# Optimization experiments

Hardware: AMD Instinct MI355X
Metric: run time of the kernel (lower is better)

Reference implementation:

```python
import jax, jax.numpy as jnp
import numpy as np

N_EMBED = 384
T_MAX = 256
EPS = 1e-5


def layer_norm(x, gamma, beta):
    mu = jnp.mean(x, axis=-1, keepdims=True)
    var = jnp.mean(jnp.square(x - mu), axis=-1, keepdims=True)
    return (x - mu) * jax.lax.rsqrt(var + EPS) * gamma + beta


def setup_inputs() -> dict:
    key = jax.random.key(0)
    ks = jax.random.split(key, 12)
    B, T, C = 128, 256, N_EMBED
    s = lambda fan_in: 1.0 / np.sqrt(fan_in)
    return {
        "x": jax.random.normal(ks[0], (B, T, C), dtype=jnp.float32),
        "W_attn": jax.random.uniform(ks[1], (C, 3 * C), minval=-s(C), maxval=s(C), dtype=jnp.float32),
        "b_attn": jax.random.uniform(ks[2], (3 * C,), minval=-s(C), maxval=s(C), dtype=jnp.float32),
        "W_proj": jax.random.uniform(ks[3], (C, C), minval=-s(C), maxval=s(C), dtype=jnp.float32),
        "b_proj": jax.random.uniform(ks[4], (C,), minval=-s(C), maxval=s(C), dtype=jnp.float32),
        "ln1_g": jnp.ones((C,), jnp.float32),
        "ln1_b": jnp.zeros((C,), jnp.float32),
        "ln2_g": jnp.ones((C,), jnp.float32),
        "ln2_b": jnp.zeros((C,), jnp.float32),
        "W1": jax.random.uniform(ks[5], (C, 4 * C), minval=-s(C), maxval=s(C), dtype=jnp.float32),
        "b1": jax.random.uniform(ks[6], (4 * C,), minval=-s(C), maxval=s(C), dtype=jnp.float32),
        "W2": jax.random.uniform(ks[7], (4 * C, C), minval=-s(4 * C), maxval=s(4 * C), dtype=jnp.float32),
        "b2": jax.random.uniform(ks[8], (4 * C,)[:1] and (C,), minval=-s(4 * C), maxval=s(4 * C), dtype=jnp.float32),
    }


def reference(x, W_attn, b_attn, W_proj, b_proj, ln1_g, ln1_b, ln2_g, ln2_b, W1, b1, W2, b2):
    B, T, C = x.shape
    # --- pre-LN single-head causal self-attention ---
    h = layer_norm(x, ln1_g, ln1_b)
    qkv = h @ W_attn + b_attn                      # [B,T,3C]
    q, k, v = jnp.split(qkv, 3, axis=-1)           # each [B,T,C]
    att = jnp.einsum('btc,bsc->bts', q, k) * (1.0 / jnp.sqrt(jnp.float32(C)))
    causal = jnp.tril(jnp.ones((T, T), bool))
    att = jnp.where(causal, att, -jnp.inf)
    att = jax.nn.softmax(att, axis=-1)             # dropout is identity (eval)
    y = jnp.einsum('bts,bsc->btc', att, v)
    x = x + (y @ W_proj + b_proj)
    # --- pre-LN MLP ---
    h2 = layer_norm(x, ln2_g, ln2_b)
    x = x + (jax.nn.relu(h2 @ W1 + b1) @ W2 + b2)
    return x
```

## Files before the change

kernel.cpp:

```cpp
#include <hip/hip_runtime.h>
#include <hip/hip_bf16.h>

#define C_EMB 384
#define T_SEQ 256
#define B_BATCH 128
#define M_ROWS (B_BATCH * T_SEQ)
#define QKV_LD 1152
#define BK 64

typedef __bf16 bf16_8 __attribute__((ext_vector_type(8)));
typedef float f32x4 __attribute__((ext_vector_type(4)));

__device__ __forceinline__ void load16_lds(const __bf16* g, __bf16* l) {
    __builtin_amdgcn_global_load_lds(
        (const __attribute__((address_space(1))) unsigned int*)g,
        (__attribute__((address_space(3))) unsigned int*)l, 16, 0, 0);
}

__global__ __launch_bounds__(256) void cast_all_kernel(const float* __restrict__ Wa,
                                                       const float* __restrict__ Wp,
                                                       const float* __restrict__ W1,
                                                       const float* __restrict__ W2,
                                                       __bf16* __restrict__ Wa_t,
                                                       __bf16* __restrict__ Wp_t,
                                                       __bf16* __restrict__ W1_t,
                                                       __bf16* __restrict__ W2_t) {
    int bid = blockIdx.x;
    const float* W; __bf16* Wt; int K, N, tx_n;
    if (bid < 432)      { W = Wa; Wt = Wa_t; K = 384;  N = 1152; tx_n = 36; }
    else if (bid < 576) { bid -= 432; W = Wp; Wt = Wp_t; K = 384;  N = 384;  tx_n = 12; }
    else if (bid < 1152){ bid -= 576; W = W1; Wt = W1_t; K = 384;  N = 1536; tx_n = 48; }
    else                { bid -= 1152; W = W2; Wt = W2_t; K = 1536; N = 384;  tx_n = 12; }
    int n0 = (bid % tx_n) * 32, k0 = (bid / tx_n) * 32;

    __shared__ float t[32][33];
    int tx = threadIdx.x & 31, ty = threadIdx.x >> 5;
#pragma unroll
    for (int i = 0; i < 4; ++i)
        t[ty + i * 8][tx] = W[(size_t)(k0 + ty + i * 8) * N + n0 + tx];
    __syncthreads();
#pragma unroll
    for (int i = 0; i < 4; ++i) {
        int n = ty + i * 8;
        Wt[(size_t)(n0 + n) * K + k0 + tx] = (__bf16)t[tx][n];
    }
}

__global__ __launch_bounds__(384) void ln_kernel(const float* __restrict__ x,
                                                 const float* __restrict__ g,
                                                 const float* __restrict__ bta,
                                                 __bf16* __restrict__ out) {
    int row = blockIdx.x;
    int c = threadIdx.x;
    float v = x[(size_t)row * C_EMB + c];

    __shared__ float red[6];
    float s = v;
#pragma unroll
    for (int o = 32; o; o >>= 1) s += __shfl_down(s, o);
    if ((c & 63) == 0) red[c >> 6] = s;
    __syncthreads();
    float mu = (red[0] + red[1] + red[2] + red[3] + red[4] + red[5]) * (1.0f / C_EMB);

    float d = v - mu;
    float s2 = d * d;
#pragma unroll
    for (int o = 32; o; o >>= 1) s2 += __shfl_down(s2, o);
    __syncthreads();
    if ((c & 63) == 0) red[c >> 6] = s2;
    __syncthreads();
    float var = (red[0] + red[1] + red[2] + red[3] + red[4] + red[5]) * (1.0f / C_EMB);

    out[(size_t)row * C_EMB + c] = (__bf16)(d * rsqrtf(var + 1e-5f) * g[c] + bta[c]);
}

template <int TM, bool RELU, bool RESID, bool OUT_BF16>
__global__ __launch_bounds__(256) void mfma_gemm(const __bf16* __restrict__ A, int lda,
                                                 const __bf16* __restrict__ Bt, int ldb,
                                                 const float* __restrict__ bias,
                                                 const float* __restrict__ resid,
                                                 void* __restrict__ out_,
                                                 int N, int K) {
    constexpr int MI = TM / 32;
    constexpr int WROWS = TM / 2;
    __shared__ __align__(16) __bf16 As[2 * TM * 32];
    __shared__ __align__(16) __bf16 Bs[2 * 128 * 32];

    int tid = threadIdx.x;
    int wave = tid >> 6, lane = tid & 63;
    int wr = wave >> 1, wc = wave & 1;
    int quad = lane >> 4, l16 = lane & 15;
    int bm = blockIdx.y * TM, bn = blockIdx.x * 128;
    int lrow = lane >> 2, lcol = (lane & 3) * 8;

    f32x4 acc[MI][4] = {};

    for (int k0 = 0; k0 < K; k0 += BK) {
        const __bf16* Ab = A + (size_t)bm * lda + k0;
        const __bf16* Bb = Bt + (size_t)bn * ldb + k0;
#pragma unroll
        for (int p = 0; p < 2; ++p) {
#pragma unroll
            for (int i = 0; i < TM / 64; ++i) {
                int r0 = (i * 4 + wave) * 16;
                load16_lds(Ab + (size_t)(r0 + lrow) * lda + p * 32 + lcol,
                           &As[p * TM * 32 + r0 * 32]);
            }
#pragma unroll
            for (int i = 0; i < 2; ++i) {
                int r0 = (i * 4 + wave) * 16;
                load16_lds(Bb + (size_t)(r0 + lrow) * ldb + p * 32 + lcol,
                           &Bs[p * 128 * 32 + r0 * 32]);
            }
        }
        __syncthreads();

        bf16_8 af[MI][2], bf[4][2];
#pragma unroll
        for (int p = 0; p < 2; ++p) {
#pragma unroll
            for (int i = 0; i < MI; ++i)
                af[i][p] = *reinterpret_cast<const bf16_8*>(
                    &As[p * TM * 32 + (wr * WROWS + i * 16 + l16) * 32 + quad * 8]);
#pragma unroll
            for (int j = 0; j < 4; ++j)
                bf[j][p] = *reinterpret_cast<const bf16_8*>(
                    &Bs[p * 128 * 32 + (wc * 64 + j * 16 + l16) * 32 + quad * 8]);
        }
#pragma unroll
        for (int i = 0; i < MI; ++i)
#pragma unroll
            for (int j = 0; j < 4; ++j) {
                acc[i][j] = __builtin_amdgcn_mfma_f32_16x16x32_bf16(af[i][0], bf[j][0], acc[i][j], 0, 0, 0);
                acc[i][j] = __builtin_amdgcn_mfma_f32_16x16x32_bf16(af[i][1], bf[j][1], acc[i][j], 0, 0, 0);
            }
        __syncthreads();
    }

#pragma unroll
    for (int i = 0; i < MI; ++i) {
#pragma unroll
        for (int r = 0; r < 4; ++r) {
            int m = bm + wr * WROWS + i * 16 + quad * 4 + r;
#pragma unroll
            for (int j = 0; j < 4; ++j) {
                int n = bn + wc * 64 + j * 16 + l16;
                float v = acc[i][j][r] + bias[n];
                if (RELU) v = fmaxf(v, 0.0f);
                if (RESID) v += resid[(size_t)m * N + n];
                if (OUT_BF16)
                    ((__bf16*)out_)[(size_t)m * N + n] = (__bf16)v;
                else
                    ((float*)out_)[(size_t)m * N + n] = v;
            }
        }
    }
}

__global__ __launch_bounds__(256) void proj_ln_kernel(const __bf16* __restrict__ A,
                                                      const __bf16* __restrict__ Bt,
                                                      const float* __restrict__ bias,
                                                      const float* __restrict__ resid,
                                                      const float* __restrict__ lng,
                                                      const float* __restrict__ lnb,
                                                      float* __restrict__ out,
                                                      __bf16* __restrict__ h) {
    __shared__ __align__(16) __bf16 As[2 * 64 * 32];
    __shared__ __align__(16) __bf16 Bs[2 * 384 * 32];
    __shared__ float red[2][2][64];

    int tid = threadIdx.x;
    int wave = tid >> 6, lane = tid & 63;
    int wr = wave >> 1, wc = wave & 1;
    int quad = lane >> 4, l16 = lane & 15;
    int bm = blockIdx.x * 64;
    int lrow = lane >> 2, lcol = (lane & 3) * 8;

    f32x4 acc[2][12] = {};

    for (int k0 = 0; k0 < C_EMB; k0 += BK) {
        const __bf16* Ab = A + (size_t)bm * C_EMB + k0;
        const __bf16* Bb = Bt + k0;
#pragma unroll
        for (int p = 0; p < 2; ++p) {
            {
                int r0 = wave * 16;
                load16_lds(Ab + (size_t)(r0 + lrow) * C_EMB + p * 32 + lcol,
                           &As[p * 64 * 32 + r0 * 32]);
            }
#pragma unroll
            for (int i = 0; i < 6; ++i) {
                int r0 = (i * 4 + wave) * 16;
                load16_lds(Bb + (size_t)(r0 + lrow) * C_EMB + p * 32 + lcol,
                           &Bs[p * 384 * 32 + r0 * 32]);
            }
        }
        __syncthreads();

        bf16_8 af[2][2], bf[12][2];
#pragma unroll
        for (int p = 0; p < 2; ++p) {
#pragma unroll
            for (int i = 0; i < 2; ++i)
                af[i][p] = *reinterpret_cast<const bf16_8*>(
                    &As[p * 64 * 32 + (wr * 32 + i * 16 + l16) * 32 + quad * 8]);
#pragma unroll
            for (int j = 0; j < 12; ++j)
                bf[j][p] = *reinterpret_cast<const bf16_8*>(
                    &Bs[p * 384 * 32 + (wc * 192 + j * 16 + l16) * 32 + quad * 8]);
        }
#pragma unroll
        for (int i = 0; i < 2; ++i)
#pragma unroll
            for (int j = 0; j < 12; ++j) {
                acc[i][j] = __builtin_amdgcn_mfma_f32_16x16x32_bf16(af[i][0], bf[j][0], acc[i][j], 0, 0, 0);
                acc[i][j] = __builtin_amdgcn_mfma_f32_16x16x32_bf16(af[i][1], bf[j][1], acc[i][j], 0, 0, 0);
            }
        __syncthreads();
    }

    float bia[12], gg[12], bb[12];
#pragma unroll
    for (int j = 0; j < 12; ++j) {
        int n = wc * 192 + j * 16 + l16;
        bia[j] = bias[n];
        gg[j] = lng[n];
        bb[j] = lnb[n];
    }

#pragma unroll
    for (int i = 0; i < 2; ++i)
#pragma unroll
        for (int r = 0; r < 4; ++r) {
            int rloc = wr * 32 + i * 16 + quad * 4 + r;
            int m = bm + rloc;
            float s = 0.0f, s2 = 0.0f;
#pragma unroll
            for (int j = 0; j < 12; ++j) {
                int n = wc * 192 + j * 16 + l16;
                float v = acc[i][j][r] + bia[j] + resid[(size_t)m * C_EMB + n];
                acc[i][j][r] = v;
                s += v;
                s2 += v * v;
            }
#pragma unroll
            for (int o = 8; o; o >>= 1) {
                s += __shfl_xor(s, o);
                s2 += __shfl_xor(s2, o);
            }
            if (l16 == 0) {
                red[0][wc][rloc] = s;
                red[1][wc][rloc] = s2;
            }
        }
    __syncthreads();

#pragma unroll
    for (int i = 0; i < 2; ++i)
#pragma unroll
        for (int r = 0; r < 4; ++r) {
            int rloc = wr * 32 + i * 16 + quad * 4 + r;
            int m = bm + rloc;
            float mu  = (red[0][0][rloc] + red[0][1][rloc]) * (1.0f / C_EMB);
            float ex2 = (red[1][0][rloc] + red[1][1][rloc]) * (1.0f / C_EMB);
            float rstd = rsqrtf(ex2 - mu * mu + 1e-5f);
#pragma unroll
            for (int j = 0; j < 12; ++j) {
                int n = wc * 192 + j * 16 + l16;
                float v = acc[i][j][r];
                out[(size_t)m * C_EMB + n] = v;
                h[(size_t)m * C_EMB + n] = (__bf16)((v - mu) * rstd * gg[j] + bb[j]);
            }
        }
}

__global__ __launch_bounds__(256) void vt_kernel(const __bf16* __restrict__ qkv,
                                                 __bf16* __restrict__ Vt) {
    __shared__ __align__(16) __bf16 t[32][72];
    int b = blockIdx.z, c0 = blockIdx.x * 64, s0 = blockIdx.y * 32;
    int tid = threadIdx.x;

    int tx = tid & 7, ty = tid >> 3;
    const __bf16* src = qkv + ((size_t)b * T_SEQ + s0 + ty) * QKV_LD + 768 + c0 + tx * 8;
    *reinterpret_cast<float4*>(&t[ty][tx * 8]) = *reinterpret_cast<const float4*>(src);
    __syncthreads();

    int sx = tid & 3, cy = tid >> 2;
    __align__(16) __bf16 tmp[8];
#pragma unroll
    for (int j = 0; j < 8; ++j) tmp[j] = t[sx * 8 + j][cy];
    *reinterpret_cast<float4*>(&Vt[((size_t)b * C_EMB + c0 + cy) * T_SEQ + s0 + sx * 8]) =
        *reinterpret_cast<float4*>(tmp);
}

__global__ __launch_bounds__(256) void qks_mfma(const __bf16* __restrict__ qkv,
                                                __bf16* __restrict__ P) {
    int b = blockIdx.y;
    int bx = blockIdx.x;
    int bm = bx * 128;
    int ntiles = bx + 1;
    const __bf16* Ab0 = qkv + (size_t)b * T_SEQ * QKV_LD;
    const __bf16* Bb0 = Ab0 + 384;

    __shared__ __align__(16) __bf16 As[2 * 128 * 32];
    __shared__ __align__(16) __bf16 Bs[2 * 128 * 32];
    __shared__ float red[2][2][128];

    int tid = threadIdx.x;
    int wave = tid >> 6, lane = tid & 63;
    int wr = wave >> 1, wc = wave & 1;
    int quad = lane >> 4, l16 = lane & 15;
    int lrow = lane >> 2, lcol = (lane & 3) * 8;

    f32x4 acc[2][4][4] = {};

#pragma unroll
    for (int nt = 0; nt < 2; ++nt) {
        if (nt < ntiles) {
            int bn = nt * 128;
            for (int k0 = 0; k0 < C_EMB; k0 += BK) {
                const __bf16* Ab = Ab0 + (size_t)bm * QKV_LD + k0;
                const __bf16* Bb = Bb0 + (size_t)bn * QKV_LD + k0;
#pragma unroll
                for (int p = 0; p < 2; ++p)
#pragma unroll
                    for (int i = 0; i < 2; ++i) {
                        int r0 = (i * 4 + wave) * 16;
                        load16_lds(Ab + (size_t)(r0 + lrow) * QKV_LD + p * 32 + lcol,
                                   &As[p * 128 * 32 + r0 * 32]);
                        load16_lds(Bb + (size_t)(r0 + lrow) * QKV_LD + p * 32 + lcol,
                                   &Bs[p * 128 * 32 + r0 * 32]);
                    }
                __syncthreads();

                bf16_8 af[4][2], bf[4][2];
#pragma unroll
                for (int p = 0; p < 2; ++p)
#pragma unroll
                    for (int i = 0; i < 4; ++i) {
                        af[i][p] = *reinterpret_cast<const bf16_8*>(
                            &As[p * 128 * 32 + (wr * 64 + i * 16 + l16) * 32 + quad * 8]);
                        bf[i][p] = *reinterpret_cast<const bf16_8*>(
                            &Bs[p * 128 * 32 + (wc * 64 + i * 16 + l16) * 32 + quad * 8]);
                    }
#pragma unroll
                for (int i = 0; i < 4; ++i)
#pragma unroll
                    for (int j = 0; j < 4; ++j) {
                        acc[nt][i][j] = __builtin_amdgcn_mfma_f32_16x16x32_bf16(af[i][0], bf[j][0], acc[nt][i][j], 0, 0, 0);
                        acc[nt][i][j] = __builtin_amdgcn_mfma_f32_16x16x32_bf16(af[i][1], bf[j][1], acc[nt][i][j], 0, 0, 0);
                    }
                __syncthreads();
            }
        }
    }

    const float scale = 0.05103103630798288f;

#pragma unroll
    for (int i = 0; i < 4; ++i)
#pragma unroll
        for (int r = 0; r < 4; ++r) {
            int rloc = wr * 64 + i * 16 + quad * 4 + r;
            int t = bm + rloc;
            float m = -INFINITY;
#pragma unroll
            for (int nt = 0; nt < 2; ++nt)
#pragma unroll
                for (int j = 0; j < 4; ++j) {
                    int n = nt * 128 + wc * 64 + j * 16 + l16;
                    bool ok = (nt < ntiles) && (n <= t);
                    float v = acc[nt][i][j][r] * scale;
                    m = fmaxf(m, ok ? v : -INFINITY);
                }
#pragma unroll
            for (int o = 8; o; o >>= 1) m = fmaxf(m, __shfl_xor(m, o));
            if (l16 == 0) red[0][wc][rloc] = m;
        }
    __syncthreads();

#pragma unroll
    for (int i = 0; i < 4; ++i)
#pragma unroll
        for (int r = 0; r < 4; ++r) {
            int rloc = wr * 64 + i * 16 + quad * 4 + r;
            int t = bm + rloc;
            float M = fmaxf(red[0][0][rloc], red[0][1][rloc]);
            float s = 0.0f;
#pragma unroll
            for (int nt = 0; nt < 2; ++nt)
#pragma unroll
                for (int j = 0; j < 4; ++j) {
                    int n = nt * 128 + wc * 64 + j * 16 + l16;
                    bool ok = (nt < ntiles) && (n <= t);
                    float p = ok ? __expf(acc[nt][i][j][r] * scale - M) : 0.0f;
                    acc[nt][i][j][r] = p;
                    s += p;
                }
#pragma unroll
            for (int o = 8; o; o >>= 1) s += __shfl_xor(s, o);
            if (l16 == 0) red[1][wc][rloc] = s;
        }
    __syncthreads();

    __bf16* Pb_ = P + (size_t)b * T_SEQ * T_SEQ;
#pragma unroll
    for (int i = 0; i < 4; ++i)
#pragma unroll
        for (int r = 0; r < 4; ++r) {
            int rloc = wr * 64 + i * 16 + quad * 4 + r;
            float inv = 1.0f / (red[1][0][rloc] + red[1][1][rloc]);
#pragma unroll
            for (int nt = 0; nt < 2; ++nt)
                if (nt < ntiles)
#pragma unroll
                    for (int j = 0; j < 4; ++j) {
                        int n = nt * 128 + wc * 64 + j * 16 + l16;
                        Pb_[(size_t)(bm + rloc) * T_SEQ + n] = (__bf16)(acc[nt][i][j][r] * inv);
                    }
        }
}

__global__ __launch_bounds__(256) void pv_mfma(const __bf16* __restrict__ P,
                                               const __bf16* __restrict__ Vt,
                                               __bf16* __restrict__ y) {
    int b = blockIdx.z;
    int bm = blockIdx.y * 128, bn = blockIdx.x * 128;
    const __bf16* Ab0 = P + (size_t)b * T_SEQ * T_SEQ;
    const __bf16* Bb0 = Vt + (size_t)b * C_EMB * T_SEQ;

    __shared__ __align__(16) __bf16 As[2 * 128 * 32];
    __shared__ __align__(16) __bf16 Bs[2 * 128 * 32];

    int tid = threadIdx.x;
    int wave = tid >> 6, lane = tid & 63;
    int wr = wave >> 1, wc = wave & 1;
    int quad = lane >> 4, l16 = lane & 15;
    int lrow = lane >> 2, lcol = (lane & 3) * 8;

    f32x4 acc[4][4] = {};

    int kmax = bm + 128;
    for (int k0 = 0; k0 < kmax; k0 += BK) {
        const __bf16* Ab = Ab0 + (size_t)bm * T_SEQ + k0;
        const __bf16* Bb = Bb0 + (size_t)bn * T_SEQ + k0;
#pragma unroll
        for (int p = 0; p < 2; ++p)
#pragma unroll
            for (int i = 0; i < 2; ++i) {
                int r0 = (i * 4 + wave) * 16;
                load16_lds(Ab + (size_t)(r0 + lrow) * T_SEQ + p * 32 + lcol,
                           &As[p * 128 * 32 + r0 * 32]);
                load16_lds(Bb + (size_t)(r0 + lrow) * T_SEQ + p * 32 + lcol,
                           &Bs[p * 128 * 32 + r0 * 32]);
            }
        __syncthreads();

        bf16_8 af[4][2], bf[4][2];
#pragma unroll
        for (int p = 0; p < 2; ++p)
#pragma unroll
            for (int i = 0; i < 4; ++i) {
                af[i][p] = *reinterpret_cast<const bf16_8*>(
                    &As[p * 128 * 32 + (wr * 64 + i * 16 + l16) * 32 + quad * 8]);
                bf[i][p] = *reinterpret_cast<const bf16_8*>(
                    &Bs[p * 128 * 32 + (wc * 64 + i * 16 + l16) * 32 + quad * 8]);
            }
#pragma unroll
        for (int i = 0; i < 4; ++i)
#pragma unroll
            for (int j = 0; j < 4; ++j) {
                acc[i][j] = __builtin_amdgcn_mfma_f32_16x16x32_bf16(af[i][0], bf[j][0], acc[i][j], 0, 0, 0);
                acc[i][j] = __builtin_amdgcn_mfma_f32_16x16x32_bf16(af[i][1], bf[j][1], acc[i][j], 0, 0, 0);
            }
        __syncthreads();
    }

#pragma unroll
    for (int i = 0; i < 4; ++i) {
#pragma unroll
        for (int r = 0; r < 4; ++r) {
            int m = bm + wr * 64 + i * 16 + quad * 4 + r;
#pragma unroll
            for (int j = 0; j < 4; ++j) {
                int n = bn + wc * 64 + j * 16 + l16;
                y[((size_t)b * T_SEQ + m) * C_EMB + n] = (__bf16)acc[i][j][r];
            }
        }
    }
}

extern "C" void kernel_launch(void* const* d_in, const int* in_sizes, int n_in,
                              void* d_out, int out_size, void* d_ws, size_t ws_size,
                              hipStream_t stream) {
    const float* x      = (const float*)d_in[0];
    const float* W_attn = (const float*)d_in[1];
    const float* b_attn = (const float*)d_in[2];
    const float* W_proj = (const float*)d_in[3];
    const float* b_proj = (const float*)d_in[4];
    const float* ln1_g  = (const float*)d_in[5];
    const float* ln1_b  = (const float*)d_in[6];
    const float* ln2_g  = (const float*)d_in[7];
    const float* ln2_b  = (const float*)d_in[8];
    const float* W1     = (const float*)d_in[9];
    const float* b1     = (const float*)d_in[10];
    const float* W2     = (const float*)d_in[11];
    const float* b2     = (const float*)d_in[12];
    float* out = (float*)d_out;

    __bf16* Wattn_t = (__bf16*)d_ws;
    __bf16* Wproj_t = Wattn_t + (size_t)1152 * 384;
    __bf16* W1_t    = Wproj_t + (size_t)384 * 384;
    __bf16* W2_t    = W1_t + (size_t)1536 * 384;
    __bf16* h       = W2_t + (size_t)384 * 1536;
    __bf16* yb      = h + (size_t)M_ROWS * 384;
    __bf16* qkv     = yb + (size_t)M_ROWS * 384;
    float*  S       = (float*)(qkv + (size_t)M_ROWS * QKV_LD);
    __bf16* Pb      = (__bf16*)(S + (size_t)B_BATCH * T_SEQ * T_SEQ);
    __bf16* Vt      = Pb + (size_t)B_BATCH * T_SEQ * T_SEQ;
    __bf16* ff      = qkv;

    cast_all_kernel<<<1728, 256, 0, stream>>>(W_attn, W_proj, W1, W2,
                                              Wattn_t, Wproj_t, W1_t, W2_t);

    ln_kernel<<<M_ROWS, 384, 0, stream>>>(x, ln1_g, ln1_b, h);
    mfma_gemm<128, false, false, true><<<dim3(1152 / 128, M_ROWS / 128), 256, 0, stream>>>(
        h, 384, Wattn_t, 384, b_attn, nullptr, qkv, 1152, 384);
    vt_kernel<<<dim3(C_EMB / 64, T_SEQ / 32, B_BATCH), 256, 0, stream>>>(qkv, Vt);
    qks_mfma<<<dim3(2, B_BATCH), 256, 0, stream>>>(qkv, Pb);
    pv_mfma<<<dim3(C_EMB / 128, T_SEQ / 128, B_BATCH), 256, 0, stream>>>(Pb, Vt, yb);
    proj_ln_kernel<<<M_ROWS / 64, 256, 0, stream>>>(yb, Wproj_t, b_proj, x,
                                                    ln2_g, ln2_b, out, h);
    mfma_gemm<128, true, false, true><<<dim3(1536 / 128, M_ROWS / 128), 256, 0, stream>>>(
        h, 384, W1_t, 384, b1, nullptr, ff, 1536, 384);
    mfma_gemm<64, false, true, false><<<dim3(384 / 128, M_ROWS / 64), 256, 0, stream>>>(
        ff, 1536, W2_t, 1536, b2, out, out, 384, 1536);
}
```

Before: 469.9 us.

## Replace GEMM kernel with double-buffered 128x384 tile pipelined MFMA GEMM

Replaces the generic MFMA GEMM with a 512-thread kernel that computes 128x384 output tiles. It double-buffers LDS so global-to-LDS loads for the next K step overlap the MFMAs on the current one, and it XOR-swizzles the LDS layout to avoid bank conflicts. Each block reuses a wider B tile, which cuts A re-reads and uses one barrier per K step. The cost is heavy LDS use (about 128KB), which limits occupancy to one block per CU, plus a large register footprint, and the W2 GEMM launches only 256 blocks.

```diff
diff --git a/kernel.cpp b/kernel.cpp
--- a/kernel.cpp
+++ b/kernel.cpp
@@ -74,87 +74,95 @@
     out[(size_t)row * C_EMB + c] = (__bf16)(d * rsqrtf(var + 1e-5f) * g[c] + bta[c]);
 }
 
-template <int TM, bool RELU, bool RESID, bool OUT_BF16>
-__global__ __launch_bounds__(256) void mfma_gemm(const __bf16* __restrict__ A, int lda,
-                                                 const __bf16* __restrict__ Bt, int ldb,
-                                                 const float* __restrict__ bias,
-                                                 const float* __restrict__ resid,
-                                                 void* __restrict__ out_,
-                                                 int N, int K) {
-    constexpr int MI = TM / 32;
-    constexpr int WROWS = TM / 2;
-    __shared__ __align__(16) __bf16 As[2 * TM * 32];
-    __shared__ __align__(16) __bf16 Bs[2 * 128 * 32];
+template <int K, int NFULL, bool RELU, bool ACCUM>
+__global__ __launch_bounds__(512, 1) void gemm_pipe(const __bf16* __restrict__ A,
+                                                    const __bf16* __restrict__ Bt,
+                                                    const float* __restrict__ bias,
+                                                    void* __restrict__ out_) {
+    __shared__ __align__(16) __bf16 At[2][128 * 64];
+    __shared__ __align__(16) __bf16 Bs[2][384 * 64];
 
     int tid = threadIdx.x;
     int wave = tid >> 6, lane = tid & 63;
-    int wr = wave >> 1, wc = wave & 1;
+    int wr = wave >> 2, wc = wave & 3;
     int quad = lane >> 4, l16 = lane & 15;
-    int bm = blockIdx.y * TM, bn = blockIdx.x * 128;
-    int lrow = lane >> 2, lcol = (lane & 3) * 8;
-
-    f32x4 acc[MI][4] = {};
-
-    for (int k0 = 0; k0 < K; k0 += BK) {
-        const __bf16* Ab = A + (size_t)bm * lda + k0;
-        const __bf16* Bb = Bt + (size_t)bn * ldb + k0;
-#pragma unroll
-        for (int p = 0; p < 2; ++p) {
-#pragma unroll
-            for (int i = 0; i < TM / 64; ++i) {
-                int r0 = (i * 4 + wave) * 16;
-                load16_lds(Ab + (size_t)(r0 + lrow) * lda + p * 32 + lcol,
-                           &As[p * TM * 32 + r0 * 32]);
-            }
-#pragma unroll
-            for (int i = 0; i < 2; ++i) {
-                int r0 = (i * 4 + wave) * 16;
-                load16_lds(Bb + (size_t)(r0 + lrow) * ldb + p * 32 + lcol,
-                           &Bs[p * 128 * 32 + r0 * 32]);
-            }
-        }
-        __syncthreads();
-
-        bf16_8 af[MI][2], bf[4][2];
-#pragma unroll
-        for (int p = 0; p < 2; ++p) {
-#pragma unroll
-            for (int i = 0; i < MI; ++i)
-                af[i][p] = *reinterpret_cast<const bf16_8*>(
-                    &As[p * TM * 32 + (wr * WROWS + i * 16 + l16) * 32 + quad * 8]);
-#pragma unroll
-            for (int j = 0; j < 4; ++j)
-                bf[j][p] = *reinterpret_cast<const bf16_8*>(
-                    &Bs[p * 128 * 32 + (wc * 64 + j * 16 + l16) * 32 + quad * 8]);
-        }
-#pragma unroll
-        for (int i = 0; i < MI; ++i)
-#pragma unroll
-            for (int j = 0; j < 4; ++j) {
-                acc[i][j] = __builtin_amdgcn_mfma_f32_16x16x32_bf16(af[i][0], bf[j][0], acc[i][j], 0, 0, 0);
-                acc[i][j] = __builtin_amdgcn_mfma_f32_16x16x32_bf16(af[i][1], bf[j][1], acc[i][j], 0, 0, 0);
-            }
-        __syncthreads();
-    }
-
-#pragma unroll
-    for (int i = 0; i < MI; ++i) {
-#pragma unroll
-        for (int r = 0; r < 4; ++r) {
-            int m = bm + wr * WROWS + i * 16 + quad * 4 + r;
-#pragma unroll
-            for (int j = 0; j < 4; ++j) {
-                int n = bn + wc * 64 + j * 16 + l16;
+    int bm = blockIdx.y * 128;
+    int n0 = blockIdx.x * 384;
+    int srow = lane >> 3;
+    int sunit = (lane & 7) ^ srow;
+
+    const __bf16* asrc0 = A + (size_t)(bm + srow) * K + sunit * 8;
+    const __bf16* bsrc0 = Bt + (size_t)(n0 + srow) * K + sunit * 8;
+
+    auto stage = [&](int buf, int k0) {
+#pragma unroll
+        for (int t = 0; t < 2; ++t) {
+            int g = t * 8 + wave;
+            load16_lds(asrc0 + (size_t)(g * 8) * K + k0, &At[buf][g * 8 * 64]);
+        }
+#pragma unroll
+        for (int t = 0; t < 6; ++t) {
+            int g = t * 8 + wave;
+            load16_lds(bsrc0 + (size_t)(g * 8) * K + k0, &Bs[buf][g * 8 * 64]);
+        }
+    };
+
+    f32x4 acc[4][6] = {};
+
+    stage(0, 0);
+    asm volatile("s_waitcnt vmcnt(0)" ::: "memory");
+    __builtin_amdgcn_sched_barrier(0);
+    __builtin_amdgcn_s_barrier();
+
+#pragma unroll 2
+    for (int kt = 0; kt < K / BK; ++kt) {
+        int cur = kt & 1;
+        if (kt < K / BK - 1) stage(cur ^ 1, (kt + 1) * BK);
+
+        bf16_8 af[4][2];
+#pragma unroll
+        for (int p = 0; p < 2; ++p)
+#pragma unroll
+            for (int i = 0; i < 4; ++i) {
+                int row = wr * 64 + i * 16 + l16;
+                int u = (p * 4 + quad) ^ (row & 7);
+                af[i][p] = *reinterpret_cast<const bf16_8*>(&At[cur][row * 64 + u * 8]);
+            }
+#pragma unroll
+        for (int p = 0; p < 2; ++p)
+#pragma unroll
+            for (int j = 0; j < 6; ++j) {
+                int row = wc * 96 + j * 16 + l16;
+                int u = (p * 4 + quad) ^ (row & 7);
+                bf16_8 bf = *reinterpret_cast<const bf16_8*>(&Bs[cur][row * 64 + u * 8]);
+#pragma unroll
+                for (int i = 0; i < 4; ++i)
+                    acc[i][j] = __builtin_amdgcn_mfma_f32_16x16x32_bf16(af[i][p], bf, acc[i][j], 0, 0, 0);
+            }
+
+        asm volatile("s_waitcnt vmcnt(0)" ::: "memory");
+        __builtin_amdgcn_sched_barrier(0);
+        __builtin_amdgcn_s_barrier();
+    }
+
+#pragma unroll
+    for (int i = 0; i < 4; ++i)
+#pragma unroll
+        for (int r = 0; r < 4; ++r) {
+            int m = bm + wr * 64 + i * 16 + quad * 4 + r;
+#pragma unroll
+            for (int j = 0; j < 6; ++j) {
+                int n = n0 + wc * 96 + j * 16 + l16;
                 float v = acc[i][j][r] + bias[n];
                 if (RELU) v = fmaxf(v, 0.0f);
-                if (RESID) v += resid[(size_t)m * N + n];
-                if (OUT_BF16)
-                    ((__bf16*)out_)[(size_t)m * N + n] = (__bf16)v;
-                else
-                    ((float*)out_)[(size_t)m * N + n] = v;
-            }
-        }
-    }
+                if (ACCUM) {
+                    float* o = &((float*)out_)[(size_t)m * NFULL + n];
+                    *o = *o + v;
+                } else {
+                    ((__bf16*)out_)[(size_t)m * NFULL + n] = (__bf16)v;
+                }
+            }
+        }
 }
 
 __global__ __launch_bounds__(256) void proj_ln_kernel(const __bf16* __restrict__ A,
@@ -524,15 +532,15 @@
                                               Wattn_t, Wproj_t, W1_t, W2_t);
 
     ln_kernel<<<M_ROWS, 384, 0, stream>>>(x, ln1_g, ln1_b, h);
-    mfma_gemm<128, false, false, true><<<dim3(1152 / 128, M_ROWS / 128), 256, 0, stream>>>(
-        h, 384, Wattn_t, 384, b_attn, nullptr, qkv, 1152, 384);
+    gemm_pipe<384, 1152, false, false><<<dim3(1152 / 384, M_ROWS / 128), 512, 0, stream>>>(
+        h, Wattn_t, b_attn, qkv);
     vt_kernel<<<dim3(C_EMB / 64, T_SEQ / 32, B_BATCH), 256, 0, stream>>>(qkv, Vt);
     qks_mfma<<<dim3(2, B_BATCH), 256, 0, stream>>>(qkv, Pb);
     pv_mfma<<<dim3(C_EMB / 128, T_SEQ / 128, B_BATCH), 256, 0, stream>>>(Pb, Vt, yb);
     proj_ln_kernel<<<M_ROWS / 64, 256, 0, stream>>>(yb, Wproj_t, b_proj, x,
                                                     ln2_g, ln2_b, out, h);
-    mfma_gemm<128, true, false, true><<<dim3(1536 / 128, M_ROWS / 128), 256, 0, stream>>>(
-        h, 384, W1_t, 384, b1, nullptr, ff, 1536, 384);
-    mfma_gemm<64, false, true, false><<<dim3(384 / 128, M_ROWS / 64), 256, 0, stream>>>(
-        ff, 1536, W2_t, 1536, b2, out, out, 384, 1536);
-}
+    gemm_pipe<384, 1536, true, false><<<dim3(1536 / 384, M_ROWS / 128), 512, 0, stream>>>(
+        h, W1_t, b1, ff);
+    gemm_pipe<1536, 384, false, true><<<dim3(1, M_ROWS / 128), 512, 0, stream>>>(
+        ff, W2_t, b2, out);
+}
```

Result: no change. 470.7 us (+0.2%).
